# Kernel tuning notes

Hardware: AMD Instinct MI355X
Metric: run time of the kernel (lower is better)

The kernel has to match this reference:

```python
import jax, jax.numpy as jnp
import numpy as np

RES = 64
NU = 0.002
DX = 2.0 * np.pi / RES
DT = 0.001
M1 = 12
M2 = 12
WIDTH = 32


def _central(x, axis, dx):
    # periodic central difference via roll (matches torch.roll semantics)
    return (jnp.roll(x, -1, axis) - jnp.roll(x, 1, axis)) / (2.0 * dx)


def _grad_module(u):
    # TurbulenceRCLN.compute_grad_u: central diff in x,y; j==2 branch is u*0.1 (kept faithfully)
    g0 = _central(u, 2, DX)
    g1 = _central(u, 3, DX)
    g2 = u * 0.1
    return jnp.stack([g0, g1, g2], axis=2)  # (B,3,3,N,N,N) indexed [b,i,j]


def _grad_solver(u):
    # NavierStokesSolver._compute_gradient: true central differences in all 3 dirs
    return jnp.stack([_central(u, 2 + j, DX) for j in range(3)], axis=2)


def _laplacian(u):
    lap = jnp.zeros_like(u)
    for ax in (2, 3, 4):
        lap = lap + (jnp.roll(u, -1, ax) - 2.0 * u + jnp.roll(u, 1, ax)) / (DX * DX)
    return lap


def _div_tau(tau):
    # tau: (B,3,3,N,N,N); div_i = sum_j d tau_ij / dx_j
    return sum(_central(tau[:, :, j], 2 + j, DX) for j in range(3))


def _spectral_conv(x, w1, w2):
    # x: (B,C,N,N); w1/w2: (C,C,M1,M2,2) real/imag
    N = x.shape[-1]
    xft = jnp.fft.rfft2(x)  # (B,C,N,N//2+1) complex
    w1c = w1[..., 0] + 1j * w1[..., 1]
    w2c = w2[..., 0] + 1j * w2[..., 1]
    a = jnp.einsum('bixy,ioxy->boxy', xft[:, :, :M1, :M2], w1c)
    b = jnp.einsum('bixy,ioxy->boxy', xft[:, :, -M1:, :M2], w2c)
    out = jnp.zeros_like(xft).at[:, :, :M1, :M2].set(a).at[:, :, -M1:, :M2].set(b)
    return jnp.fft.irfft2(out, s=(N, N))


def _fno2d(x, fc0_w, fc0_b, spec_w1, spec_w2, conv_w, conv_b, fc1_w, fc1_b, fc2_w, fc2_b):
    h = jnp.einsum('bcxy,cd->bdxy', x, fc0_w) + fc0_b[None, :, None, None]
    for l in range(4):
        s = _spectral_conv(h, spec_w1[l], spec_w2[l])
        w = jnp.einsum('bcxy,co->boxy', h, conv_w[l]) + conv_b[l][None, :, None, None]
        h = s + w
        if l < 3:
            h = jax.nn.gelu(h)
    h = jax.nn.gelu(jnp.einsum('bcxy,cd->bdxy', h, fc1_w) + fc1_b[None, :, None, None])
    return jnp.einsum('bcxy,cd->bdxy', h, fc2_w) + fc2_b[None, :, None, None]


def setup_inputs() -> dict:
    key = jax.random.key(0)
    ks = jax.random.split(key, 8)
    B = 16
    scale = 1.0 / (WIDTH * WIDTH)
    return {
        'velocity': jax.random.normal(ks[0], (B, 3, RES, RES, RES), jnp.float32),
        'fc0_w': jax.random.normal(ks[1], (10, WIDTH), jnp.float32) * 0.1,
        'fc0_b': jnp.zeros((WIDTH,), jnp.float32),
        'spec_w1': jax.random.normal(ks[2], (4, WIDTH, WIDTH, M1, M2, 2), jnp.float32) * scale,
        'spec_w2': jax.random.normal(ks[3], (4, WIDTH, WIDTH, M1, M2, 2), jnp.float32) * scale,
        'conv_w': jax.random.normal(ks[4], (4, WIDTH, WIDTH), jnp.float32) * 0.1,
        'conv_b': jnp.zeros((4, WIDTH), jnp.float32),
        'fc1_w': jax.random.normal(ks[5], (WIDTH, 128), jnp.float32) * 0.1,
        'fc1_b': jnp.zeros((128,), jnp.float32),
        'fc2_w': jax.random.normal(ks[6], (128, 6), jnp.float32) * 0.1,
        'fc2_b': jnp.zeros((6,), jnp.float32),
    }


def reference(velocity, fc0_w, fc0_b, spec_w1, spec_w2, conv_w, conv_b, fc1_w, fc1_b, fc2_w, fc2_b):
    B = velocity.shape[0]
    N = RES
    # --- soft-shell closure input ---
    grad_u = _grad_module(velocity)                                   # (B,3,3,N,N,N)
    S = 0.5 * (grad_u + jnp.swapaxes(grad_u, 1, 2))
    S_mag = jnp.sqrt(2.0 * jnp.sum(S * S, axis=(1, 2), keepdims=True))  # (B,1,1,N,N,N)
    g_slice = grad_u[:, :, :, :, N // 2, :].reshape(B, 9, N, N)        # 9 grad channels at mid-plane
    s_slice = S_mag[:, :, :, :, N // 2, :].reshape(B, 1, N, N)         # 1 strain-mag channel
    closure_in = jnp.concatenate([g_slice, s_slice], axis=1)          # (B,10,N,N)
    tau2d = _fno2d(closure_in, fc0_w, fc0_b, spec_w1, spec_w2, conv_w, conv_b,
                   fc1_w, fc1_b, fc2_w, fc2_b)                         # (B,6,N,N)
    t = jnp.broadcast_to(tau2d[..., None], (B, 6, N, N, N))           # expand along z
    # reconstruct symmetric stress tensor (B,3,3,N,N,N)
    row0 = jnp.stack([t[:, 0], t[:, 3], t[:, 4]], axis=1)
    row1 = jnp.stack([t[:, 3], t[:, 1], t[:, 5]], axis=1)
    row2 = jnp.stack([t[:, 4], t[:, 5], t[:, 2]], axis=1)
    tau_full = jnp.stack([row0, row1, row2], axis=1)
    # --- hard-core NS step ---
    g = _grad_solver(velocity)
    lap = _laplacian(velocity)
    convection = jnp.einsum('bixyz,bijxyz->bjxyz', velocity, g)
    div_tau = _div_tau(tau_full)
    return velocity + DT * (-convection + NU * lap + div_tau)
```

## Files before the change

kernel.cpp:

```cpp
#include <hip/hip_runtime.h>
#include <math.h>

#define NRES 64
#define NXY  4096
#define NVOL 262144
#define BB   16
#define WID  32
#define MM   12
#define R24  24

constexpr double DX_d   = 2.0 * 3.14159265358979323846 / 64.0;
constexpr float  INV2DX = (float)(1.0 / (2.0 * DX_d));
constexpr float  INVDX2 = (float)(1.0 / (DX_d * DX_d));
constexpr float  DT_c   = 0.001f;
constexpr float  NU_c   = 0.002f;

constexpr size_t OFF_FR  = 0;
constexpr size_t OFF_FI  = OFF_FR + (size_t)R24 * NRES;
constexpr size_t OFF_GR  = OFF_FI + (size_t)R24 * NRES;
constexpr size_t OFF_GI  = OFF_GR + (size_t)MM * NRES;
constexpr size_t OFF_CL  = OFF_GI + (size_t)MM * NRES;
constexpr size_t OFF_HA  = OFF_CL + (size_t)BB * 10 * NXY;
constexpr size_t OFF_HB  = OFF_HA + (size_t)BB * WID * NXY;
constexpr size_t OFF_T1R = OFF_HB + (size_t)BB * WID * NXY;
constexpr size_t OFF_T1I = OFF_T1R + (size_t)BB * WID * R24 * NRES;
constexpr size_t OFF_XR  = OFF_T1I + (size_t)BB * WID * R24 * NRES;
constexpr size_t OFF_XI  = OFF_XR + (size_t)BB * WID * R24 * MM;
constexpr size_t OFF_MR  = OFF_XI + (size_t)BB * WID * R24 * MM;
constexpr size_t OFF_MI  = OFF_MR + (size_t)BB * WID * R24 * MM;
constexpr size_t OFF_AR  = OFF_MI + (size_t)BB * WID * R24 * MM;
constexpr size_t OFF_AI  = OFF_AR + (size_t)BB * WID * MM * NRES;
constexpr size_t OFF_H1  = OFF_AI + (size_t)BB * WID * MM * NRES;
constexpr size_t OFF_TAU = OFF_H1 + (size_t)BB * 128 * NXY;
constexpr size_t OFF_FRT = OFF_TAU + (size_t)BB * 6 * NXY;
constexpr size_t OFF_FIT = OFF_FRT + (size_t)NRES * R24;

constexpr size_t OFF_SP  = OFF_H1;
constexpr size_t OFF_W1T = OFF_H1 + (size_t)BB * WID * NXY;
constexpr size_t OFF_CWT = OFF_W1T + 4096;
constexpr size_t OFF_W0T = OFF_CWT + 4096;

__device__ __forceinline__ float gelu_fast(float x) {
    float z = 0.79788456080286535588f * (x + 0.044715f * x * x * x);
    float e = __expf(2.0f * z);
    float t = 1.0f - 2.0f / (e + 1.0f);
    return 0.5f * x * (1.0f + t);
}

__device__ __forceinline__ float2 gelu2(float2 v) {
    return make_float2(gelu_fast(v.x), gelu_fast(v.y));
}

__global__ void k_setup(const float* __restrict__ fc1w, const float* __restrict__ convw,
                        const float* __restrict__ fc0w, float* __restrict__ ws) {
    int idx = blockIdx.x * 256 + threadIdx.x;
    if (idx < R24 * NRES) {
        int r = idx / NRES, x = idx % NRES;
        int kx = (r < MM) ? r : (r + 40);
        double ang = -2.0 * 3.14159265358979323846 * (double)(kx * x) / 64.0;
        float cr = (float)cos(ang), ci = (float)sin(ang);
        ws[OFF_FR + idx] = cr;
        ws[OFF_FI + idx] = ci;
        ws[OFF_FRT + (size_t)x * R24 + r] = cr;
        ws[OFF_FIT + (size_t)x * R24 + r] = ci;
    }
    if (idx < MM * NRES) {
        int ky = idx / NRES, y = idx % NRES;
        double ang = -2.0 * 3.14159265358979323846 * (double)(ky * y) / 64.0;
        ws[OFF_GR + idx] = (float)cos(ang);
        ws[OFF_GI + idx] = (float)sin(ang);
    }
    if (idx < 4096) {
        int c = idx >> 7, e = idx & 127;
        ws[OFF_W1T + (size_t)e * 32 + c] = fc1w[idx];
    } else if (idx < 8192) {
        int j = idx - 4096;
        int l = j >> 10, r = j & 1023;
        int c = r >> 5, o = r & 31;
        ws[OFF_CWT + (size_t)l * 1024 + o * 32 + c] = convw[j];
    } else if (idx < 8512) {
        int j = idx - 8192;
        int c = j >> 5, d = j & 31;
        ws[OFF_W0T + (size_t)d * 10 + c] = fc0w[j];
    }
}

__global__ void k_clfc0(const float* __restrict__ v, const float* __restrict__ w0t,
                        const float* __restrict__ bias, float* __restrict__ h) {
    __shared__ __align__(16) float sw[32 * 12];
    __shared__ float sb[32];
    int tid = threadIdx.x;
    for (int i = tid; i < 320; i += 256) {
        int d = i / 10, c = i % 10;
        sw[d * 12 + c] = w0t[i];
    }
    if (tid < 32) sb[tid] = bias[tid];
    __syncthreads();
    int idx = blockIdx.x * 256 + tid;
    int b = idx >> 10;
    int rr = idx & 1023;
    int x = rr >> 4, z0 = (rr & 15) * 4;
    int xp = (x + 1) & 63, xm = (x - 1) & 63;
    float4 cv[10];
    for (int i = 0; i < 3; i++) {
        const float* vb = v + (((size_t)(b * 3 + i)) << 18);
        float4 u4   = *(const float4*)(vb + (size_t)x  * 4096 + 32 * 64 + z0);
        float4 uxp4 = *(const float4*)(vb + (size_t)xp * 4096 + 32 * 64 + z0);
        float4 uxm4 = *(const float4*)(vb + (size_t)xm * 4096 + 32 * 64 + z0);
        float4 uyp4 = *(const float4*)(vb + (size_t)x  * 4096 + 33 * 64 + z0);
        float4 uym4 = *(const float4*)(vb + (size_t)x  * 4096 + 31 * 64 + z0);
        cv[i * 3 + 0] = make_float4((uxp4.x - uxm4.x) * INV2DX, (uxp4.y - uxm4.y) * INV2DX,
                                    (uxp4.z - uxm4.z) * INV2DX, (uxp4.w - uxm4.w) * INV2DX);
        cv[i * 3 + 1] = make_float4((uyp4.x - uym4.x) * INV2DX, (uyp4.y - uym4.y) * INV2DX,
                                    (uyp4.z - uym4.z) * INV2DX, (uyp4.w - uym4.w) * INV2DX);
        cv[i * 3 + 2] = make_float4(0.1f * u4.x, 0.1f * u4.y, 0.1f * u4.z, 0.1f * u4.w);
    }
    float4 ss = make_float4(0.f, 0.f, 0.f, 0.f);
    for (int i = 0; i < 3; i++)
        for (int j = 0; j < 3; j++) {
            float4 a = cv[i * 3 + j], bt = cv[j * 3 + i];
            float sx = 0.5f * (a.x + bt.x), sy = 0.5f * (a.y + bt.y);
            float sz = 0.5f * (a.z + bt.z), sw_ = 0.5f * (a.w + bt.w);
            ss.x += sx * sx; ss.y += sy * sy; ss.z += sz * sz; ss.w += sw_ * sw_;
        }
    cv[9] = make_float4(sqrtf(2.f * ss.x), sqrtf(2.f * ss.y),
                        sqrtf(2.f * ss.z), sqrtf(2.f * ss.w));
    float* hp = h + (size_t)b * WID * NXY + (size_t)x * 64 + z0;
#pragma unroll
    for (int d = 0; d < 32; d++) {
        float4 acc = make_float4(sb[d], sb[d], sb[d], sb[d]);
#pragma unroll
        for (int c = 0; c < 10; c++) {
            float w = sw[d * 12 + c];
            acc.x += w * cv[c].x; acc.y += w * cv[c].y;
            acc.z += w * cv[c].z; acc.w += w * cv[c].w;
        }
        *(float4*)(hp + (size_t)d * NXY) = acc;
    }
}

__global__ void k_fwd(const float* __restrict__ h, const float* __restrict__ ws,
                      float* __restrict__ xr, float* __restrict__ xi) {
    __shared__ __align__(16) float sh[4096];
    __shared__ float st1r[24 * 65];
    __shared__ float st1i[24 * 65];
    int tid = threadIdx.x;
    int bc = blockIdx.x;
    const float4* hp4 = (const float4*)(h + (size_t)bc * NXY);
    float4* sh4 = (float4*)sh;
#pragma unroll
    for (int i = 0; i < 4; i++) sh4[tid + 256 * i] = hp4[tid + 256 * i];
    __syncthreads();
    const float* FRT = ws + OFF_FRT;
    const float* FIT = ws + OFF_FIT;
#pragma unroll
    for (int it = 0; it < 6; it++) {
        int point = it * 256 + tid;
        int y = point & 63;
        int rr = __builtin_amdgcn_readfirstlane(point >> 6);
        float ar = 0.f, ai = 0.f;
#pragma unroll 16
        for (int x = 0; x < 64; x++) {
            float hv = sh[x * 64 + y];
            ar += hv * FRT[x * R24 + rr];
            ai += hv * FIT[x * R24 + rr];
        }
        st1r[rr * 65 + y] = ar;
        st1i[rr * 65 + y] = ai;
    }
    __syncthreads();
    const float* GR = ws + OFF_GR;
    const float* GI = ws + OFF_GI;
#pragma unroll
    for (int it = 0; it < 2; it++) {
        int point = it * 256 + tid;
        if (point < 288) {
            int r = point / 12, ky = point - r * 12;
            const float* Gr = GR + (size_t)ky * 64;
            const float* Gi = GI + (size_t)ky * 64;
            float ar = 0.f, ai = 0.f;
#pragma unroll 16
            for (int y = 0; y < 64; y++) {
                float a = st1r[r * 65 + y], b = st1i[r * 65 + y];
                float c = Gr[y], d = Gi[y];
                ar += a * c - b * d;
                ai += a * d + b * c;
            }
            xr[(size_t)bc * 288 + point] = ar;
            xi[(size_t)bc * 288 + point] = ai;
        }
    }
}

__global__ void k_specinv(const float* __restrict__ xr, const float* __restrict__ xi,
                          const float* __restrict__ w1, const float* __restrict__ w2,
                          const float* __restrict__ ws, float* __restrict__ sp) {
    __shared__ float sm_r[288];
    __shared__ float sm_i[288];
    __shared__ float sa_r[12 * 64];
    __shared__ float sa_i[12 * 64];
    int tid = threadIdx.x;
    int bo = blockIdx.x;
    int o = bo & 31, b = bo >> 5;
    for (int m = tid; m < 288; m += 256) {
        int r = m / 12;
        int kxy = (r < MM) ? m : (m - 144);
        const float* wp = ((r < MM) ? w1 : w2) + ((size_t)o * 144 + kxy) * 2;
        size_t xbase = (size_t)b * 32 * 288 + m;
        float ar = 0.f, ai = 0.f;
#pragma unroll 8
        for (int i = 0; i < 32; i++) {
            float a   = xr[xbase + (size_t)i * 288];
            float bb  = xi[xbase + (size_t)i * 288];
            float wr_ = wp[(size_t)i * 9216];
            float wi_ = wp[(size_t)i * 9216 + 1];
            ar += a * wr_ - bb * wi_;
            ai += a * wi_ + bb * wr_;
        }
        sm_r[m] = ar; sm_i[m] = ai;
    }
    __syncthreads();
    const float* FR = ws + OFF_FR;
    const float* FI = ws + OFF_FI;
#pragma unroll
    for (int it = 0; it < 3; it++) {
        int point = it * 256 + tid;
        int x = point & 63;
        int ky = __builtin_amdgcn_readfirstlane(point >> 6);
        float ar = 0.f, ai = 0.f;
#pragma unroll 8
        for (int r = 0; r < 24; r++) {
            float a = sm_r[r * 12 + ky], bb = sm_i[r * 12 + ky];
            float c = FR[r * 64 + x], d = FI[r * 64 + x];
            ar += a * c + bb * d;
            ai += bb * c - a * d;
        }
        sa_r[ky * 64 + x] = ar;
        sa_i[ky * 64 + x] = ai;
    }
    __syncthreads();
    const float* GR = ws + OFF_GR;
    const float* GI = ws + OFF_GI;
    float* spb = sp + (size_t)bo * NXY;
#pragma unroll
    for (int it = 0; it < 16; it++) {
        int px = it * 256 + tid;
        int y = px & 63;
        int x = __builtin_amdgcn_readfirstlane(px >> 6);
        float s = sa_r[x];
#pragma unroll
        for (int ky = 1; ky < 12; ky++) {
            float gr = GR[ky * 64 + y];
            float gi = GI[ky * 64 + y];
            s += 2.0f * (sa_r[ky * 64 + x] * gr + sa_i[ky * 64 + x] * gi);
        }
        spb[px] = s * (1.0f / 4096.0f);
    }
}

template <int DOGELU>
__global__ void k_convg(const float* __restrict__ sp, const float* __restrict__ hin,
                        const float* __restrict__ cwt, const float* __restrict__ cb,
                        float* __restrict__ hout) {
    __shared__ __align__(16) float scw[1024];
    __shared__ float scb[32];
    int tid = threadIdx.x;
#pragma unroll
    for (int i = 0; i < 4; i++) scw[tid + 256 * i] = cwt[tid + 256 * i];
    if (tid < 32) scb[tid] = cb[tid];
    __syncthreads();
    int wid = tid >> 6, lane = tid & 63;
    int pix = blockIdx.x * 64 + lane;
    int b = pix >> 12, p = pix & 4095;
    const float* hp = hin + (size_t)b * WID * NXY + p;
    float hv[32];
#pragma unroll
    for (int c = 0; c < 32; c++) hv[c] = hp[(size_t)c * NXY];
    const float* spp = sp + (size_t)b * WID * NXY + p;
    float* op = hout + (size_t)b * WID * NXY + p;
#pragma unroll
    for (int j = 0; j < 8; j++) {
        int o = wid * 8 + j;
        const float4* wr = (const float4*)&scw[o * 32];
        float a0 = 0.f, a1 = 0.f, a2 = 0.f, a3 = 0.f;
#pragma unroll
        for (int q = 0; q < 8; q += 4) {
            float4 w0 = wr[q], w1 = wr[q + 1], w2 = wr[q + 2], w3 = wr[q + 3];
            a0 += w0.x * hv[q * 4]      + w0.y * hv[q * 4 + 1]  + w0.z * hv[q * 4 + 2]  + w0.w * hv[q * 4 + 3];
            a1 += w1.x * hv[q * 4 + 4]  + w1.y * hv[q * 4 + 5]  + w1.z * hv[q * 4 + 6]  + w1.w * hv[q * 4 + 7];
            a2 += w2.x * hv[q * 4 + 8]  + w2.y * hv[q * 4 + 9]  + w2.z * hv[q * 4 + 10] + w2.w * hv[q * 4 + 11];
            a3 += w3.x * hv[q * 4 + 12] + w3.y * hv[q * 4 + 13] + w3.z * hv[q * 4 + 14] + w3.w * hv[q * 4 + 15];
        }
        float v = scb[o] + (a0 + a1) + (a2 + a3) + spp[(size_t)o * NXY];
        if (DOGELU) v = gelu_fast(v);
        op[(size_t)o * NXY] = v;
    }
}

__global__ void __launch_bounds__(256, 2)
k_head(const float* __restrict__ h, const float* __restrict__ w1t,
       const float* __restrict__ b1, const float* __restrict__ w2,
       const float* __restrict__ b2, float* __restrict__ tau) {
    __shared__ __align__(16) float sw1[4096];
    __shared__ float sb1[128];
    __shared__ __align__(16) float sw2[128 * 8];
    __shared__ __align__(8) float2 red[4][6][64];
    int tid = threadIdx.x;
#pragma unroll
    for (int i = 0; i < 16; i++) sw1[tid + 256 * i] = w1t[tid + 256 * i];
    if (tid < 128) sb1[tid] = b1[tid];
    for (int i = tid; i < 768; i += 256) {
        int e = i / 6, t = i - e * 6;
        sw2[e * 8 + t] = w2[i];
    }
    __syncthreads();
    int wid = tid >> 6, lane = tid & 63;
    int q = blockIdx.x * 64 + lane;
    int b = q >> 11, p = (q & 2047) * 2;
    const float* hp = h + (size_t)b * WID * NXY + p;
    float2 hv[32];
#pragma unroll
    for (int c = 0; c < 32; c++) hv[c] = *(const float2*)(hp + (size_t)c * NXY);
    float2 acc[6];
#pragma unroll
    for (int t = 0; t < 6; t++) acc[t] = make_float2(0.f, 0.f);
#pragma unroll 4
    for (int jj = 0; jj < 32; jj++) {
        int e = wid * 32 + jj;
        const float4* wr = (const float4*)&sw1[e * 32];
        float2 d = make_float2(sb1[e], sb1[e]);
#pragma unroll
        for (int q8 = 0; q8 < 8; q8++) {
            float4 w = wr[q8];
            float2 h0 = hv[q8 * 4], h1 = hv[q8 * 4 + 1], h2 = hv[q8 * 4 + 2], h3 = hv[q8 * 4 + 3];
            d.x += w.x * h0.x + w.y * h1.x + w.z * h2.x + w.w * h3.x;
            d.y += w.x * h0.y + w.y * h1.y + w.z * h2.y + w.w * h3.y;
        }
        float2 g = gelu2(d);
        const float4* w2r = (const float4*)&sw2[e * 8];
        float4 wa = w2r[0], wb = w2r[1];
        acc[0].x += g.x * wa.x; acc[0].y += g.y * wa.x;
        acc[1].x += g.x * wa.y; acc[1].y += g.y * wa.y;
        acc[2].x += g.x * wa.z; acc[2].y += g.y * wa.z;
        acc[3].x += g.x * wa.w; acc[3].y += g.y * wa.w;
        acc[4].x += g.x * wb.x; acc[4].y += g.y * wb.x;
        acc[5].x += g.x * wb.y; acc[5].y += g.y * wb.y;
    }
#pragma unroll
    for (int t = 0; t < 6; t++) red[wid][t][lane] = acc[t];
    __syncthreads();
    if (wid == 0) {
        float* tb = tau + (size_t)b * 6 * NXY + p;
#pragma unroll
        for (int t = 0; t < 6; t++) {
            float2 r0 = red[0][t][lane], r1 = red[1][t][lane];
            float2 r2 = red[2][t][lane], r3 = red[3][t][lane];
            float bv = b2[t];
            float2 s = make_float2(r0.x + r1.x + r2.x + r3.x + bv,
                                   r0.y + r1.y + r2.y + r3.y + bv);
            *(float2*)(tb + (size_t)t * NXY) = s;
        }
    }
}

__global__ void __launch_bounds__(256, 2)
k_ns(const float* __restrict__ v, const float* __restrict__ tau,
     float* __restrict__ out) {
    int idx = blockIdx.x * 256 + threadIdx.x;
    int b = idx >> 16;
    int r = idx & 65535;
    int x = r >> 10;
    int y = (r >> 4) & 63;
    int z0 = (r & 15) * 4;
    int xp = (x + 1) & 63, xm = (x - 1) & 63;
    int yp = (y + 1) & 63, ym = (y - 1) & 63;
    int zm = (z0 - 1) & 63, zp = (z0 + 4) & 63;

    float4 u[3], gx[3], gy[3], gz[3], lap[3];
    for (int i = 0; i < 3; i++) {
        const float* vb = v + (((size_t)(b * 3 + i)) << 18);
        const float* row = vb + (size_t)x * 4096 + (size_t)y * 64;
        float4 c4   = *(const float4*)(row + z0);
        float  czm  = row[zm];
        float  czp  = row[zp];
        float4 xp4  = *(const float4*)(vb + (size_t)xp * 4096 + (size_t)y * 64 + z0);
        float4 xm4  = *(const float4*)(vb + (size_t)xm * 4096 + (size_t)y * 64 + z0);
        float4 yp4  = *(const float4*)(vb + (size_t)x * 4096 + (size_t)yp * 64 + z0);
        float4 ym4  = *(const float4*)(vb + (size_t)x * 4096 + (size_t)ym * 64 + z0);
        u[i] = c4;
        gx[i] = make_float4((xp4.x - xm4.x) * INV2DX, (xp4.y - xm4.y) * INV2DX,
                            (xp4.z - xm4.z) * INV2DX, (xp4.w - xm4.w) * INV2DX);
        gy[i] = make_float4((yp4.x - ym4.x) * INV2DX, (yp4.y - ym4.y) * INV2DX,
                            (yp4.z - ym4.z) * INV2DX, (yp4.w - ym4.w) * INV2DX);
        gz[i] = make_float4((c4.y - czm) * INV2DX, (c4.z - c4.x) * INV2DX,
                            (c4.w - c4.y) * INV2DX, (czp - c4.z) * INV2DX);
        lap[i] = make_float4(
            (xp4.x + xm4.x + yp4.x + ym4.x + czm  + c4.y - 6.f * c4.x) * INVDX2,
            (xp4.y + xm4.y + yp4.y + ym4.y + c4.x + c4.z - 6.f * c4.y) * INVDX2,
            (xp4.z + xm4.z + yp4.z + ym4.z + c4.y + c4.w - 6.f * c4.z) * INVDX2,
            (xp4.w + xm4.w + yp4.w + ym4.w + c4.z + czp  - 6.f * c4.w) * INVDX2);
    }
    const float* tb = tau + (size_t)b * 6 * NXY;
    int pxp = xp * 64 + y, pxm = xm * 64 + y, pyp = x * 64 + yp, pym = x * 64 + ym;
    float d0 = (tb[0 * NXY + pxp] - tb[0 * NXY + pxm]) * INV2DX +
               (tb[3 * NXY + pyp] - tb[3 * NXY + pym]) * INV2DX;
    float d1 = (tb[3 * NXY + pxp] - tb[3 * NXY + pxm]) * INV2DX +
               (tb[1 * NXY + pyp] - tb[1 * NXY + pym]) * INV2DX;
    float d2 = (tb[4 * NXY + pxp] - tb[4 * NXY + pxm]) * INV2DX +
               (tb[5 * NXY + pyp] - tb[5 * NXY + pym]) * INV2DX;

    size_t so = ((size_t)b * 3) * NVOL + (size_t)x * 4096 + (size_t)y * 64 + z0;
#pragma unroll
    for (int i = 0; i < 3; i++) {
        float dti = (i == 0) ? d0 : (i == 1) ? d1 : d2;
        float4 conv = make_float4(
            u[0].x * ((i==0)?gx[0].x:(i==1)?gy[0].x:gz[0].x) + u[1].x * ((i==0)?gx[1].x:(i==1)?gy[1].x:gz[1].x) + u[2].x * ((i==0)?gx[2].x:(i==1)?gy[2].x:gz[2].x),
            u[0].y * ((i==0)?gx[0].y:(i==1)?gy[0].y:gz[0].y) + u[1].y * ((i==0)?gx[1].y:(i==1)?gy[1].y:gz[1].y) + u[2].y * ((i==0)?gx[2].y:(i==1)?gy[2].y:gz[2].y),
            u[0].z * ((i==0)?gx[0].z:(i==1)?gy[0].z:gz[0].z) + u[1].z * ((i==0)?gx[1].z:(i==1)?gy[1].z:gz[1].z) + u[2].z * ((i==0)?gx[2].z:(i==1)?gy[2].z:gz[2].z),
            u[0].w * ((i==0)?gx[0].w:(i==1)?gy[0].w:gz[0].w) + u[1].w * ((i==0)?gx[1].w:(i==1)?gy[1].w:gz[1].w) + u[2].w * ((i==0)?gx[2].w:(i==1)?gy[2].w:gz[2].w));
        float4 res = make_float4(
            u[i].x + DT_c * (-conv.x + NU_c * lap[i].x + dti),
            u[i].y + DT_c * (-conv.y + NU_c * lap[i].y + dti),
            u[i].z + DT_c * (-conv.z + NU_c * lap[i].z + dti),
            u[i].w + DT_c * (-conv.w + NU_c * lap[i].w + dti));
        *(float4*)(out + so + (size_t)i * NVOL) = res;
    }
}

extern "C" void kernel_launch(void* const* d_in, const int* in_sizes, int n_in,
                              void* d_out, int out_size, void* d_ws, size_t ws_size,
                              hipStream_t stream) {
    const float* vel   = (const float*)d_in[0];
    const float* fc0w  = (const float*)d_in[1];
    const float* fc0b  = (const float*)d_in[2];
    const float* sw1   = (const float*)d_in[3];
    const float* sw2   = (const float*)d_in[4];
    const float* convw = (const float*)d_in[5];
    const float* convb = (const float*)d_in[6];
    const float* fc1w  = (const float*)d_in[7];
    const float* fc1b  = (const float*)d_in[8];
    const float* fc2w  = (const float*)d_in[9];
    const float* fc2b  = (const float*)d_in[10];
    float* ws  = (float*)d_ws;
    float* out = (float*)d_out;

    k_setup<<<34, 256, 0, stream>>>(fc1w, convw, fc0w, ws);
    k_clfc0<<<64, 256, 0, stream>>>(vel, ws + OFF_W0T, fc0b, ws + OFF_HA);

    float* hcur  = ws + OFF_HA;
    float* hnext = ws + OFF_HB;
    for (int l = 0; l < 4; l++) {
        const float* wl1 = sw1 + (size_t)l * WID * WID * MM * MM * 2;
        const float* wl2 = sw2 + (size_t)l * WID * WID * MM * MM * 2;
        const float* cwl = ws + OFF_CWT + (size_t)l * WID * WID;
        const float* cbl = convb + (size_t)l * WID;
        k_fwd<<<512, 256, 0, stream>>>(hcur, ws, ws + OFF_XR, ws + OFF_XI);
        k_specinv<<<512, 256, 0, stream>>>(ws + OFF_XR, ws + OFF_XI, wl1, wl2, ws, ws + OFF_SP);
        if (l < 3)
            k_convg<1><<<1024, 256, 0, stream>>>(ws + OFF_SP, hcur, cwl, cbl, hnext);
        else
            k_convg<0><<<1024, 256, 0, stream>>>(ws + OFF_SP, hcur, cwl, cbl, hnext);
        float* tmp = hcur; hcur = hnext; hnext = tmp;
    }

    k_head<<<512, 256, 0, stream>>>(hcur, ws + OFF_W1T, fc1b, fc2w, fc2b, ws + OFF_TAU);
    k_ns<<<4096, 256, 0, stream>>>(vel, ws + OFF_TAU, out);
}
```

Baseline: 247.3 us.

## Split FNO forward-DFT, conv and head kernels across more blocks for occupancy

The forward DFT kernel is split into two blocks per channel, each handling half of the retained x-frequency rows. The 1x1 conv kernel now processes pixel pairs and splits output channels across two blocks. The head kernel splits its 128 hidden units across two blocks, writes partial results, and adds a small reduction kernel that sums them and applies the bias. The aim is more parallelism and less per-block serial work, at the cost of reloading the input tiles twice and an extra launch plus partial-sum traffic.

```diff
diff --git a/kernel.cpp b/kernel.cpp
--- a/kernel.cpp
+++ b/kernel.cpp
@@ -39,6 +39,8 @@
 constexpr size_t OFF_W1T = OFF_H1 + (size_t)BB * WID * NXY;
 constexpr size_t OFF_CWT = OFF_W1T + 4096;
 constexpr size_t OFF_W0T = OFF_CWT + 4096;
+constexpr size_t OFF_PT  = OFF_T1R;
+constexpr size_t PT_STRIDE = (size_t)BB * 6 * NXY;
 
 __device__ __forceinline__ float gelu_fast(float x) {
     float z = 0.79788456080286535588f * (x + 0.044715f * x * x * x);
@@ -142,10 +144,12 @@
 __global__ void k_fwd(const float* __restrict__ h, const float* __restrict__ ws,
                       float* __restrict__ xr, float* __restrict__ xi) {
     __shared__ __align__(16) float sh[4096];
-    __shared__ float st1r[24 * 65];
-    __shared__ float st1i[24 * 65];
+    __shared__ float st1r[12 * 65];
+    __shared__ float st1i[12 * 65];
     int tid = threadIdx.x;
-    int bc = blockIdx.x;
+    int blk = blockIdx.x;
+    int bc = blk >> 1, half = blk & 1;
+    int rbase = half * 12;
     const float4* hp4 = (const float4*)(h + (size_t)bc * NXY);
     float4* sh4 = (float4*)sh;
 #pragma unroll
@@ -154,41 +158,39 @@
     const float* FRT = ws + OFF_FRT;
     const float* FIT = ws + OFF_FIT;
 #pragma unroll
-    for (int it = 0; it < 6; it++) {
+    for (int it = 0; it < 3; it++) {
         int point = it * 256 + tid;
         int y = point & 63;
-        int rr = __builtin_amdgcn_readfirstlane(point >> 6);
+        int rl = __builtin_amdgcn_readfirstlane(point >> 6);
+        int rg = rbase + rl;
         float ar = 0.f, ai = 0.f;
 #pragma unroll 16
         for (int x = 0; x < 64; x++) {
             float hv = sh[x * 64 + y];
-            ar += hv * FRT[x * R24 + rr];
-            ai += hv * FIT[x * R24 + rr];
-        }
-        st1r[rr * 65 + y] = ar;
-        st1i[rr * 65 + y] = ai;
+            ar += hv * FRT[x * R24 + rg];
+            ai += hv * FIT[x * R24 + rg];
+        }
+        st1r[rl * 65 + y] = ar;
+        st1i[rl * 65 + y] = ai;
     }
     __syncthreads();
     const float* GR = ws + OFF_GR;
     const float* GI = ws + OFF_GI;
-#pragma unroll
-    for (int it = 0; it < 2; it++) {
-        int point = it * 256 + tid;
-        if (point < 288) {
-            int r = point / 12, ky = point - r * 12;
-            const float* Gr = GR + (size_t)ky * 64;
-            const float* Gi = GI + (size_t)ky * 64;
-            float ar = 0.f, ai = 0.f;
+    if (tid < 144) {
+        int rl = tid / 12, ky = tid - rl * 12;
+        const float* Gr = GR + (size_t)ky * 64;
+        const float* Gi = GI + (size_t)ky * 64;
+        float ar = 0.f, ai = 0.f;
 #pragma unroll 16
-            for (int y = 0; y < 64; y++) {
-                float a = st1r[r * 65 + y], b = st1i[r * 65 + y];
-                float c = Gr[y], d = Gi[y];
-                ar += a * c - b * d;
-                ai += a * d + b * c;
-            }
-            xr[(size_t)bc * 288 + point] = ar;
-            xi[(size_t)bc * 288 + point] = ai;
-        }
+        for (int yy = 0; yy < 64; yy++) {
+            float a = st1r[rl * 65 + yy], b = st1i[rl * 65 + yy];
+            float c = Gr[yy], d = Gi[yy];
+            ar += a * c - b * d;
+            ai += a * d + b * c;
+        }
+        size_t outp = (size_t)bc * 288 + (size_t)(rbase + rl) * 12 + ky;
+        xr[outp] = ar;
+        xi[outp] = ai;
     }
 }
 
@@ -259,9 +261,10 @@
 }
 
 template <int DOGELU>
-__global__ void k_convg(const float* __restrict__ sp, const float* __restrict__ hin,
-                        const float* __restrict__ cwt, const float* __restrict__ cb,
-                        float* __restrict__ hout) {
+__global__ void __launch_bounds__(256, 2)
+k_convg(const float* __restrict__ sp, const float* __restrict__ hin,
+        const float* __restrict__ cwt, const float* __restrict__ cb,
+        float* __restrict__ hout) {
     __shared__ __align__(16) float scw[1024];
     __shared__ float scb[32];
     int tid = threadIdx.x;
@@ -270,65 +273,21 @@
     if (tid < 32) scb[tid] = cb[tid];
     __syncthreads();
     int wid = tid >> 6, lane = tid & 63;
-    int pix = blockIdx.x * 64 + lane;
-    int b = pix >> 12, p = pix & 4095;
+    int blk = blockIdx.x;
+    int osec = blk & 1;
+    int q = (blk >> 1) * 64 + lane;
+    int b = q >> 11, p = (q & 2047) * 2;
     const float* hp = hin + (size_t)b * WID * NXY + p;
-    float hv[32];
-#pragma unroll
-    for (int c = 0; c < 32; c++) hv[c] = hp[(size_t)c * NXY];
+    float2 hv[32];
+#pragma unroll
+    for (int c = 0; c < 32; c++) hv[c] = *(const float2*)(hp + (size_t)c * NXY);
     const float* spp = sp + (size_t)b * WID * NXY + p;
     float* op = hout + (size_t)b * WID * NXY + p;
 #pragma unroll
-    for (int j = 0; j < 8; j++) {
-        int o = wid * 8 + j;
+    for (int j = 0; j < 4; j++) {
+        int o = osec * 16 + wid * 4 + j;
         const float4* wr = (const float4*)&scw[o * 32];
-        float a0 = 0.f, a1 = 0.f, a2 = 0.f, a3 = 0.f;
-#pragma unroll
-        for (int q = 0; q < 8; q += 4) {
-            float4 w0 = wr[q], w1 = wr[q + 1], w2 = wr[q + 2], w3 = wr[q + 3];
-            a0 += w0.x * hv[q * 4]      + w0.y * hv[q * 4 + 1]  + w0.z * hv[q * 4 + 2]  + w0.w * hv[q * 4 + 3];
-            a1 += w1.x * hv[q * 4 + 4]  + w1.y * hv[q * 4 + 5]  + w1.z * hv[q * 4 + 6]  + w1.w * hv[q * 4 + 7];
-            a2 += w2.x * hv[q * 4 + 8]  + w2.y * hv[q * 4 + 9]  + w2.z * hv[q * 4 + 10] + w2.w * hv[q * 4 + 11];
-            a3 += w3.x * hv[q * 4 + 12] + w3.y * hv[q * 4 + 13] + w3.z * hv[q * 4 + 14] + w3.w * hv[q * 4 + 15];
-        }
-        float v = scb[o] + (a0 + a1) + (a2 + a3) + spp[(size_t)o * NXY];
-        if (DOGELU) v = gelu_fast(v);
-        op[(size_t)o * NXY] = v;
-    }
-}
-
-__global__ void __launch_bounds__(256, 2)
-k_head(const float* __restrict__ h, const float* __restrict__ w1t,
-       const float* __restrict__ b1, const float* __restrict__ w2,
-       const float* __restrict__ b2, float* __restrict__ tau) {
-    __shared__ __align__(16) float sw1[4096];
-    __shared__ float sb1[128];
-    __shared__ __align__(16) float sw2[128 * 8];
-    __shared__ __align__(8) float2 red[4][6][64];
-    int tid = threadIdx.x;
-#pragma unroll
-    for (int i = 0; i < 16; i++) sw1[tid + 256 * i] = w1t[tid + 256 * i];
-    if (tid < 128) sb1[tid] = b1[tid];
-    for (int i = tid; i < 768; i += 256) {
-        int e = i / 6, t = i - e * 6;
-        sw2[e * 8 + t] = w2[i];
-    }
-    __syncthreads();
-    int wid = tid >> 6, lane = tid & 63;
-    int q = blockIdx.x * 64 + lane;
-    int b = q >> 11, p = (q & 2047) * 2;
-    const float* hp = h + (size_t)b * WID * NXY + p;
-    float2 hv[32];
-#pragma unroll
-    for (int c = 0; c < 32; c++) hv[c] = *(const float2*)(hp + (size_t)c * NXY);
-    float2 acc[6];
-#pragma unroll
-    for (int t = 0; t < 6; t++) acc[t] = make_float2(0.f, 0.f);
-#pragma unroll 4
-    for (int jj = 0; jj < 32; jj++) {
-        int e = wid * 32 + jj;
-        const float4* wr = (const float4*)&sw1[e * 32];
-        float2 d = make_float2(sb1[e], sb1[e]);
+        float2 d = make_float2(scb[o], scb[o]);
 #pragma unroll
         for (int q8 = 0; q8 < 8; q8++) {
             float4 w = wr[q8];
@@ -336,8 +295,57 @@
             d.x += w.x * h0.x + w.y * h1.x + w.z * h2.x + w.w * h3.x;
             d.y += w.x * h0.y + w.y * h1.y + w.z * h2.y + w.w * h3.y;
         }
+        float2 spv = *(const float2*)(spp + (size_t)o * NXY);
+        float2 v2 = make_float2(d.x + spv.x, d.y + spv.y);
+        if (DOGELU) v2 = gelu2(v2);
+        *(float2*)(op + (size_t)o * NXY) = v2;
+    }
+}
+
+__global__ void __launch_bounds__(256, 2)
+k_head(const float* __restrict__ h, const float* __restrict__ w1t,
+       const float* __restrict__ b1, const float* __restrict__ w2,
+       float* __restrict__ pt) {
+    __shared__ __align__(16) float sw1[64 * 32];
+    __shared__ float sb1l[64];
+    __shared__ __align__(16) float sw2l[64 * 8];
+    __shared__ __align__(8) float2 red[4][6][64];
+    int tid = threadIdx.x;
+    int blk = blockIdx.x;
+    int esec = blk & 1;
+    int ebase = esec * 64;
+#pragma unroll
+    for (int i = 0; i < 8; i++) sw1[tid + 256 * i] = w1t[(size_t)ebase * 32 + tid + 256 * i];
+    if (tid < 64) sb1l[tid] = b1[ebase + tid];
+    for (int i = tid; i < 384; i += 256) {
+        int e = i / 6, t = i - e * 6;
+        sw2l[e * 8 + t] = w2[(size_t)(ebase + e) * 6 + t];
+    }
+    __syncthreads();
+    int wid = tid >> 6, lane = tid & 63;
+    int q = (blk >> 1) * 64 + lane;
+    int b = q >> 11, p = (q & 2047) * 2;
+    const float* hp = h + (size_t)b * WID * NXY + p;
+    float2 hv[32];
+#pragma unroll
+    for (int c = 0; c < 32; c++) hv[c] = *(const float2*)(hp + (size_t)c * NXY);
+    float2 acc[6];
+#pragma unroll
+    for (int t = 0; t < 6; t++) acc[t] = make_float2(0.f, 0.f);
+#pragma unroll 4
+    for (int jj = 0; jj < 16; jj++) {
+        int el = wid * 16 + jj;
+        const float4* wr = (const float4*)&sw1[el * 32];
+        float2 d = make_float2(sb1l[el], sb1l[el]);
+#pragma unroll
+        for (int q8 = 0; q8 < 8; q8++) {
+            float4 w = wr[q8];
+            float2 h0 = hv[q8 * 4], h1 = hv[q8 * 4 + 1], h2 = hv[q8 * 4 + 2], h3 = hv[q8 * 4 + 3];
+            d.x += w.x * h0.x + w.y * h1.x + w.z * h2.x + w.w * h3.x;
+            d.y += w.x * h0.y + w.y * h1.y + w.z * h2.y + w.w * h3.y;
+        }
         float2 g = gelu2(d);
-        const float4* w2r = (const float4*)&sw2[e * 8];
+        const float4* w2r = (const float4*)&sw2l[el * 8];
         float4 wa = w2r[0], wb = w2r[1];
         acc[0].x += g.x * wa.x; acc[0].y += g.y * wa.x;
         acc[1].x += g.x * wa.y; acc[1].y += g.y * wa.y;
@@ -350,17 +358,23 @@
     for (int t = 0; t < 6; t++) red[wid][t][lane] = acc[t];
     __syncthreads();
     if (wid == 0) {
-        float* tb = tau + (size_t)b * 6 * NXY + p;
+        float* pb = pt + (size_t)esec * PT_STRIDE + (size_t)b * 6 * NXY + p;
 #pragma unroll
         for (int t = 0; t < 6; t++) {
             float2 r0 = red[0][t][lane], r1 = red[1][t][lane];
             float2 r2 = red[2][t][lane], r3 = red[3][t][lane];
-            float bv = b2[t];
-            float2 s = make_float2(r0.x + r1.x + r2.x + r3.x + bv,
-                                   r0.y + r1.y + r2.y + r3.y + bv);
-            *(float2*)(tb + (size_t)t * NXY) = s;
-        }
-    }
+            float2 s = make_float2(r0.x + r1.x + r2.x + r3.x,
+                                   r0.y + r1.y + r2.y + r3.y);
+            *(float2*)(pb + (size_t)t * NXY) = s;
+        }
+    }
+}
+
+__global__ void k_tred(const float* __restrict__ pt, const float* __restrict__ b2,
+                       float* __restrict__ tau) {
+    int idx = blockIdx.x * 256 + threadIdx.x;
+    int t = (idx >> 12) % 6;
+    tau[idx] = pt[idx] + pt[idx + PT_STRIDE] + b2[t];
 }
 
 __global__ void __launch_bounds__(256, 2)
@@ -454,7 +468,7 @@
         const float* wl2 = sw2 + (size_t)l * WID * WID * MM * MM * 2;
         const float* cwl = ws + OFF_CWT + (size_t)l * WID * WID;
         const float* cbl = convb + (size_t)l * WID;
-        k_fwd<<<512, 256, 0, stream>>>(hcur, ws, ws + OFF_XR, ws + OFF_XI);
+        k_fwd<<<1024, 256, 0, stream>>>(hcur, ws, ws + OFF_XR, ws + OFF_XI);
         k_specinv<<<512, 256, 0, stream>>>(ws + OFF_XR, ws + OFF_XI, wl1, wl2, ws, ws + OFF_SP);
         if (l < 3)
             k_convg<1><<<1024, 256, 0, stream>>>(ws + OFF_SP, hcur, cwl, cbl, hnext);
@@ -463,6 +477,7 @@
         float* tmp = hcur; hcur = hnext; hnext = tmp;
     }
 
-    k_head<<<512, 256, 0, stream>>>(hcur, ws + OFF_W1T, fc1b, fc2w, fc2b, ws + OFF_TAU);
+    k_head<<<1024, 256, 0, stream>>>(hcur, ws + OFF_W1T, fc1b, fc2w, ws + OFF_PT);
+    k_tred<<<1536, 256, 0, stream>>>(ws + OFF_PT, fc2b, ws + OFF_TAU);
     k_ns<<<4096, 256, 0, stream>>>(vel, ws + OFF_TAU, out);
 }
```

Measured after the change: 238.5 us. -3.5%, faster.
